# Kernel tuning notes

Hardware: AMD Instinct MI355X
Metric: run time of the kernel (lower is better)

## Reference

```python
import jax, jax.numpy as jnp
import numpy as np

PS = 8          # patch size
E = 8           # experts per layer
L = 2           # PCE layers
F = 4           # fourier frequencies -> pos channels = 2+4F = 18
TEMP = 1.0
GROUPS = 4
B, H, W, CS, NCLS = 64, 128, 128, 8, 100
P = (H // PS) * (W // PS)
N = B * P
CAP = int(np.ceil(1.25 * N / E))  # expert capacity
POSC = 2 + 4 * F


def conv3x3(x, w):
    return jax.lax.conv_general_dilated(x, w, (1, 1), 'SAME',
                                        dimension_numbers=('NCHW', 'OIHW', 'NCHW'))


def patchify(x, ps):
    b, c, h, w = x.shape
    hp, wp = h // ps, w // ps
    t = x.reshape(b, c, hp, ps, wp, ps).transpose(0, 2, 4, 1, 3, 5)
    return t.reshape(b * hp * wp, c, ps, ps), hp, wp


def unpatchify(t, b, hp, wp):
    n, c, ph, pw = t.shape
    return t.reshape(b, hp, wp, c, ph, pw).transpose(0, 3, 1, 4, 2, 5).reshape(b, c, hp * ph, wp * pw)


def fourier_pos(h, w, f):
    yy, xx = jnp.meshgrid(jnp.linspace(-1., 1., h), jnp.linspace(-1., 1., w), indexing='ij')
    feats = [yy, xx]
    for k in range(f):
        fr = jnp.pi * (2.0 ** k)
        feats += [jnp.sin(fr * yy), jnp.cos(fr * yy), jnp.sin(fr * xx), jnp.cos(fr * xx)]
    return jnp.stack(feats, 0)  # [2+4F, H, W]


def group_norm(x, s, b, groups=GROUPS, eps=1e-5):
    n, c, h, w = x.shape
    xg = x.reshape(n, groups, c // groups, h, w)
    mu = xg.mean((2, 3, 4), keepdims=True)
    var = xg.var((2, 3, 4), keepdims=True)
    xg = (xg - mu) / jnp.sqrt(var + eps)
    return xg.reshape(n, c, h, w) * s[None, :, None, None] + b[None, :, None, None]


def setup_inputs():
    key = jax.random.key(0)
    ks = jax.random.split(key, 8)
    return {
        'X': jax.random.normal(ks[0], (B, 3, H, W), jnp.float32),
        'stem_w': jax.random.normal(ks[1], (CS, 3, 3, 3), jnp.float32) * 0.1,
        'stem_scale': jnp.ones((CS,), jnp.float32),
        'stem_bias': jnp.zeros((CS,), jnp.float32),
        'gate_w': jax.random.normal(ks[2], (L, POSC, E), jnp.float32) * 0.1,
        'gate_b': jnp.zeros((L, E), jnp.float32),
        'exp_w': jax.random.normal(ks[3], (L, E, CS, CS, 3, 3), jnp.float32) * 0.05,
        'exp_b': jnp.zeros((L, E, CS), jnp.float32),
        'gn_scale': jnp.ones((L, CS), jnp.float32),
        'gn_bias': jnp.zeros((L, CS), jnp.float32),
        'head_w1': jax.random.normal(ks[4], (CS, 4 * CS), jnp.float32) * 0.1,
        'head_b1': jnp.zeros((4 * CS,), jnp.float32),
        'head_w2': jax.random.normal(ks[5], (4 * CS, NCLS), jnp.float32) * 0.1,
        'head_b2': jnp.zeros((NCLS,), jnp.float32),
    }


def reference(X, stem_w, stem_scale, stem_bias, gate_w, gate_b, exp_w, exp_b,
              gn_scale, gn_bias, head_w1, head_b1, head_w2, head_b2):
    b = X.shape[0]
    # stem: conv + (folded) BN affine + SiLU
    x = jax.nn.silu(conv3x3(X, stem_w) * stem_scale[None, :, None, None]
                    + stem_bias[None, :, None, None])
    tokens, hp, wp = patchify(x, PS)                       # [N, CS, PS, PS]
    pos = fourier_pos(x.shape[2], x.shape[3], F)           # [POSC, H, W]
    pos_p, _, _ = patchify(pos[None], PS)                  # [P, POSC, PS, PS]
    pos_pool = jnp.tile(pos_p.mean((2, 3)), (b, 1))        # [N, POSC]

    tot_z = jnp.float32(0.)
    tot_imb = jnp.float32(0.)
    for l in range(L):
        logits = pos_pool @ gate_w[l] + gate_b[l]          # [N, E]
        probs = jax.nn.softmax(logits / TEMP, axis=-1)
        tot_z = tot_z + jnp.mean(jax.nn.logsumexp(logits, axis=-1) ** 2)
        e_idx = jnp.argmax(probs, axis=-1)                 # top-1 expert per token
        oh = jax.nn.one_hot(e_idx, E, dtype=jnp.float32)
        slot = (jnp.sum(jnp.cumsum(oh, axis=0) * oh, axis=1) - 1.).astype(jnp.int32)
        keep = slot < CAP
        frac = jnp.mean(oh * keep[:, None].astype(jnp.float32), axis=0)
        tot_imb = tot_imb + E * jnp.sum(jnp.mean(probs, axis=0) * frac)
        gate = jnp.take_along_axis(probs, e_idx[:, None], axis=1)[:, 0] * keep.astype(probs.dtype)
        e_safe = jnp.where(keep, e_idx, E)                 # OOB index -> dropped
        einp = jnp.zeros((E, CAP) + tokens.shape[1:], tokens.dtype)
        einp = einp.at[e_safe, slot].set(tokens, mode='drop')   # dispatch gather
        eout = jax.vmap(lambda xi, wi, bi: jax.nn.silu(conv3x3(xi, wi)
                        + bi[None, :, None, None]))(einp, exp_w[l], exp_b[l])
        out = eout[e_idx, jnp.minimum(slot, CAP - 1)] * gate[:, None, None, None]
        if l == L - 1:
            x = group_norm(unpatchify(out, b, hp, wp), gn_scale[l], gn_bias[l])
        else:
            tokens = group_norm(out, gn_scale[l], gn_bias[l])

    pooled = x.mean((2, 3))                                # AdaptiveAvgPool2d(1)+flatten
    h1 = jax.nn.gelu(pooled @ head_w1 + head_b1)
    logits_out = h1 @ head_w2 + head_b2
    return logits_out, tot_z, tot_imb
```

## Files before the change

kernel.cpp:

```cpp
#include <hip/hip_runtime.h>
#include <math.h>

#define CAPV 2560

typedef __bf16 bf16x8 __attribute__((ext_vector_type(8)));
typedef float f32x4 __attribute__((ext_vector_type(4)));

__device__ __forceinline__ float wave_sum64(float v) {
#pragma unroll
  for (int o = 32; o; o >>= 1) v += __shfl_xor(v, o, 64);
  return v;
}

__device__ __forceinline__ float silu_f(float t) {
  return t * __builtin_amdgcn_rcpf(1.f + __expf(-t));
}

__global__ __launch_bounds__(256) void routing_kernel(
    const float* __restrict__ gate_w, const float* __restrict__ gate_b,
    const float* __restrict__ stem_w, const float* __restrict__ stem_sc,
    const float* __restrict__ exp_w,
    int* __restrict__ route_e, float* __restrict__ route_gate,
    int* __restrict__ route_cpre, int* __restrict__ route_Ce,
    __bf16* __restrict__ stemPack, __bf16* __restrict__ expPack,
    float* __restrict__ d_scalars) {
  const int tid = threadIdx.x;
  if (blockIdx.x > 0) {
    int le = blockIdx.x - 1;
    for (int i = tid; i < 1536; i += 256) {
      int c = i >> 9, rem = i & 511, ln = rem >> 3, j = rem & 7;
      int k = c * 32 + ((ln >> 4) << 3) + j;
      int cl = ln & 15;
      int tap = k >> 3, ci = k & 7;
      int dy = tap >> 2, dx = tap & 3;
      float v = 0.f;
      if (cl < 8 && dx < 3)
        v = exp_w[((le * 8 + cl) * 8 + ci) * 9 + dy * 3 + dx];
      expPack[le * 1536 + i] = (__bf16)v;
    }
    return;
  }
  for (int i = tid; i < 1536; i += 256) {
    int c = i >> 9, rem = i & 511, ln = rem >> 3, j = rem & 7;
    int k = c * 32 + ((ln >> 4) << 3) + j;
    int cl = ln & 15;
    int tap = k >> 3, ci = k & 7;
    int dy = tap >> 2, dx = tap & 3;
    float v = 0.f;
    if (cl < 8 && dx < 3 && ci < 3)
      v = stem_w[(cl * 3 + ci) * 9 + dy * 3 + dx] * stem_sc[cl];
    stemPack[i] = (__bf16)v;
  }

  __shared__ float tS[128][4], tC[128][4];
  __shared__ float sS8[16][4], sC8[16][4];
  if (tid < 128) {
    float yv = -1.f + (2.f / 127.f) * (float)tid;
#pragma unroll
    for (int k = 0; k < 4; ++k) {
      float fr = 3.14159265358979323846f * (float)(1 << k);
      tS[tid][k] = sinf(fr * yv);
      tC[tid][k] = cosf(fr * yv);
    }
  }
  __syncthreads();
  if (tid < 64) {
    int g8 = tid >> 2, k = tid & 3;
    float s = 0.f, c = 0.f;
#pragma unroll
    for (int r = 0; r < 8; ++r) {
      s += tS[g8 * 8 + r][k];
      c += tC[g8 * 8 + r][k];
    }
    sS8[g8][k] = s * 0.125f;
    sC8[g8][k] = c * 0.125f;
  }
  __syncthreads();

  const int p = tid;
  const int lane = p & 63, wv = p >> 6;
  const int hp = p >> 4, wp = p & 15;

  float pool[18];
  pool[0] = -1.f + (2.f / 127.f) * ((float)(hp * 8) + 3.5f);
  pool[1] = -1.f + (2.f / 127.f) * ((float)(wp * 8) + 3.5f);
#pragma unroll
  for (int k = 0; k < 4; ++k) {
    pool[2 + 4 * k] = sS8[hp][k];
    pool[3 + 4 * k] = sC8[hp][k];
    pool[4 + 4 * k] = sS8[wp][k];
    pool[5 + 4 * k] = sC8[wp][k];
  }

  __shared__ float sWP[4][8];
  __shared__ float sWZ[4];
  __shared__ int sWCnt[4][8];
  __shared__ float sMeanP[8], sFrac[8];
  __shared__ float sAcc[2];
  if (p == 0) { sAcc[0] = 0.f; sAcc[1] = 0.f; }

  for (int l = 0; l < 2; ++l) {
    float logit[8];
#pragma unroll
    for (int e = 0; e < 8; ++e) logit[e] = gate_b[l * 8 + e];
#pragma unroll
    for (int c = 0; c < 18; ++c) {
      float pl = pool[c];
#pragma unroll
      for (int e = 0; e < 8; ++e)
        logit[e] = fmaf(pl, gate_w[(l * 18 + c) * 8 + e], logit[e]);
    }
    float mxv = logit[0]; int em = 0;
#pragma unroll
    for (int e = 1; e < 8; ++e)
      if (logit[e] > mxv) { mxv = logit[e]; em = e; }
    float pr[8]; float se = 0.f;
#pragma unroll
    for (int e = 0; e < 8; ++e) { pr[e] = expf(logit[e] - mxv); se += pr[e]; }
    float inv = 1.f / se;
#pragma unroll
    for (int e = 0; e < 8; ++e) pr[e] *= inv;
    float lse = mxv + logf(se);
    float gate_val = inv;

    unsigned long long meq[8];
#pragma unroll
    for (int e = 0; e < 8; ++e) meq[e] = __ballot(em == e);
    unsigned long long mm = meq[0];
#pragma unroll
    for (int e = 1; e < 8; ++e) mm = (em == e) ? meq[e] : mm;
    unsigned long long below = (2ull << lane) - 1ull;
    int cpre_w = (int)__popcll(mm & below);
    if (lane < 8) {
      unsigned long long t = meq[0];
#pragma unroll
      for (int e = 1; e < 8; ++e) t = (lane == e) ? meq[e] : t;
      sWCnt[wv][lane] = (int)__popcll(t);
    }
    float z2 = wave_sum64(lse * lse);
    if (lane == 0) sWZ[wv] = z2;
#pragma unroll
    for (int e = 0; e < 8; ++e) {
      float s = wave_sum64(pr[e]);
      if (lane == 0) sWP[wv][e] = s;
    }
    __syncthreads();

    int cpre = cpre_w;
#pragma unroll
    for (int w2 = 0; w2 < 4; ++w2)
      if (w2 < wv) cpre += sWCnt[w2][em];

    route_e[l * 256 + p] = em;
    route_gate[l * 256 + p] = gate_val;
    route_cpre[l * 256 + p] = cpre;

    if (p < 8) {
      int ce = sWCnt[0][p] + sWCnt[1][p] + sWCnt[2][p] + sWCnt[3][p];
      route_Ce[l * 8 + p] = ce;
      int kept = 0;
      for (int bb = 0; bb < 64; ++bb) {
        int r = CAPV - bb * ce;
        r = r < 0 ? 0 : r;
        kept += (r < ce ? r : ce);
      }
      sFrac[p] = (float)kept * (1.f / 16384.f);
      sMeanP[p] = (sWP[0][p] + sWP[1][p] + sWP[2][p] + sWP[3][p]) * (1.f / 256.f);
    }
    __syncthreads();
    if (p == 0) {
      float s = 0.f;
#pragma unroll
      for (int e = 0; e < 8; ++e) s += sMeanP[e] * sFrac[e];
      sAcc[1] += 8.f * s;
      sAcc[0] += (sWZ[0] + sWZ[1] + sWZ[2] + sWZ[3]) * (1.f / 256.f);
    }
    __syncthreads();
  }
  if (p == 0) { d_scalars[0] = sAcc[0]; d_scalars[1] = sAcc[1]; }
}

__global__ __launch_bounds__(256) void token_kernel(
    const float* __restrict__ X,
    const __bf16* __restrict__ stemPack, const float* __restrict__ stem_bi,
    const __bf16* __restrict__ expPack, const float* __restrict__ exp_b,
    const float* __restrict__ gn_s, const float* __restrict__ gn_b,
    const int* __restrict__ route_e, const float* __restrict__ route_gate,
    const int* __restrict__ route_cpre, const int* __restrict__ route_Ce,
    float* __restrict__ blk_sums) {
  const int g = blockIdx.x;
  const int b = g >> 6, r6 = g & 63;
  const int hp = r6 >> 2, wq = r6 & 3;
  const int tid = threadIdx.x;
  const int w = tid >> 6, lane = tid & 63;
  const int p = hp * 16 + wq * 4 + w;

  const int col = lane & 15;
  const int gq = lane >> 4;
  const int ay = (lane & 15) >> 3;
  const int ax = lane & 7;
  const int dy_ = (gq >> 1) + 1, dx_ = (gq & 1) * 4 + 1;

  __shared__ __align__(16) __bf16 sH[10][36][8];
  __shared__ __align__(16) __bf16 sT[4][10][12][8];
  __shared__ float sRed[4][12];

  const int e0 = __builtin_amdgcn_readfirstlane(route_e[p]);
  const int e1 = __builtin_amdgcn_readfirstlane(route_e[256 + p]);
  const float gp0 = route_gate[p], gp1 = route_gate[256 + p];
  const int cp0 = route_cpre[p], cp1 = route_cpre[256 + p];
  const int Ce0 = route_Ce[e0], Ce1 = route_Ce[8 + e1];
  const float gate0 = (col < 8 && b * Ce0 + cp0 <= CAPV) ? gp0 : 0.f;
  const float gate1 = (col < 8 && b * Ce1 + cp1 <= CAPV) ? gp1 : 0.f;
  const int le0 = e0, le1 = 8 + e1;
  const bf16x8* sp = (const bf16x8*)stemPack;
  const bf16x8* bp0 = (const bf16x8*)(expPack + le0 * 1536);
  const bf16x8* bp1 = (const bf16x8*)(expPack + le1 * 1536);
  bf16x8 SB0 = sp[lane], SB1 = sp[64 + lane], SB2 = sp[128 + lane];
  bf16x8 B00 = bp0[lane], B01 = bp0[64 + lane], B02 = bp0[128 + lane];
  bf16x8 B10 = bp1[lane], B11 = bp1[64 + lane], B12 = bp1[128 + lane];

  {
    float4 z4 = {0.f, 0.f, 0.f, 0.f};
    float4* h4 = (float4*)&sH[0][0][0];
#pragma unroll
    for (int i = 0; i < 2; ++i) {
      int idx = tid + i * 256;
      if (idx < 360) h4[idx] = z4;
    }
  }
  if (lane < 56) {
    int row, c2;
    if (lane < 12) { row = 0; c2 = lane; }
    else if (lane < 24) { row = 9; c2 = lane - 12; }
    else { int q = lane - 24; row = 1 + (q >> 2); int m = q & 3; c2 = (m == 0) ? 0 : 8 + m; }
    int4 z = {0, 0, 0, 0};
    *(int4*)&sT[w][row][c2][0] = z;
  }
  __syncthreads();

  const int gy0 = hp * 8 - 1, gx0 = wq * 32 - 1;
#pragma unroll
  for (int k = 0; k < 4; ++k) {
    int i = tid + k * 256;
    if (i < 1020) {
      int ci = i / 340, rem = i - ci * 340;
      int r = rem / 34, c = rem - r * 34;
      int gy = gy0 + r, gx = gx0 + c;
      if (gy >= 0 && gy < 128 && gx >= 0 && gx < 128)
        sH[r][c][ci] = (__bf16)X[((b * 3 + ci) * 128 + gy) * 128 + gx];
    }
  }
  __syncthreads();

  {
    const float bias = stem_bi[col & 7];
    f32x4 d0 = {bias, bias, bias, bias};
    f32x4 d1 = d0, d2 = d0, d3 = d0;
#pragma unroll
    for (int c = 0; c < 3; ++c) {
      const __bf16* ab = &sH[ay + c][w * 8 + ax + gq][0];
      bf16x8 A0 = *(const bf16x8*)(ab);
      bf16x8 A1 = *(const bf16x8*)(ab + 576);
      bf16x8 A2 = *(const bf16x8*)(ab + 1152);
      bf16x8 A3 = *(const bf16x8*)(ab + 1728);
      bf16x8 Bc = (c == 0) ? SB0 : (c == 1) ? SB1 : SB2;
      d0 = __builtin_amdgcn_mfma_f32_16x16x32_bf16(A0, Bc, d0, 0, 0, 0);
      d1 = __builtin_amdgcn_mfma_f32_16x16x32_bf16(A1, Bc, d1, 0, 0, 0);
      d2 = __builtin_amdgcn_mfma_f32_16x16x32_bf16(A2, Bc, d2, 0, 0, 0);
      d3 = __builtin_amdgcn_mfma_f32_16x16x32_bf16(A3, Bc, d3, 0, 0, 0);
    }
    if (col < 8) {
#pragma unroll
      for (int rg = 0; rg < 4; ++rg) {
        f32x4 dr = (rg == 0) ? d0 : (rg == 1) ? d1 : (rg == 2) ? d2 : d3;
#pragma unroll
        for (int r = 0; r < 4; ++r) {
          float t = silu_f(dr[r]);
          sT[w][rg * 2 + dy_][dx_ + r][col] = (__bf16)t;
        }
      }
    }
  }

  const __bf16* abase = &sT[w][ay][ax + gq][0];
  const float bias0 = exp_b[le0 * 8 + (col & 7)];
  const float bias1 = exp_b[le1 * 8 + (col & 7)];
  const float sgs0 = gn_s[col & 7], sgb0 = gn_b[col & 7];

  float v1s, v1q;
  {
    f32x4 a0 = {bias0, bias0, bias0, bias0};
    f32x4 a1 = a0, a2 = a0, a3 = a0;
#pragma unroll
    for (int c = 0; c < 3; ++c) {
      bf16x8 A0 = *(const bf16x8*)(abase + (0 * 192 + c * 96));
      bf16x8 A1 = *(const bf16x8*)(abase + (1 * 192 + c * 96));
      bf16x8 A2 = *(const bf16x8*)(abase + (2 * 192 + c * 96));
      bf16x8 A3 = *(const bf16x8*)(abase + (3 * 192 + c * 96));
      bf16x8 Bc = (c == 0) ? B00 : (c == 1) ? B01 : B02;
      a0 = __builtin_amdgcn_mfma_f32_16x16x32_bf16(A0, Bc, a0, 0, 0, 0);
      a1 = __builtin_amdgcn_mfma_f32_16x16x32_bf16(A1, Bc, a1, 0, 0, 0);
      a2 = __builtin_amdgcn_mfma_f32_16x16x32_bf16(A2, Bc, a2, 0, 0, 0);
      a3 = __builtin_amdgcn_mfma_f32_16x16x32_bf16(A3, Bc, a3, 0, 0, 0);
    }
    float v[16];
    float s = 0.f, q = 0.f;
#pragma unroll
    for (int rg = 0; rg < 4; ++rg) {
      f32x4 ar = (rg == 0) ? a0 : (rg == 1) ? a1 : (rg == 2) ? a2 : a3;
#pragma unroll
      for (int r = 0; r < 4; ++r) {
        float t = silu_f(ar[r]) * gate0;
        v[rg * 4 + r] = t;
        s += t;
        q += t * t;
      }
    }
    s += __shfl_xor(s, 16, 64); q += __shfl_xor(q, 16, 64);
    s += __shfl_xor(s, 32, 64); q += __shfl_xor(q, 32, 64);
    s += __shfl_xor(s, 1, 64);  q += __shfl_xor(q, 1, 64);
    float mu = s * (1.f / 128.f);
    float var = q * (1.f / 128.f) - mu * mu;
    float inv = rsqrtf(var + 1e-5f);
    float sc2 = inv * sgs0;
    float bi2 = fmaf(-mu, sc2, sgb0);
    if (col < 8) {
#pragma unroll
      for (int rg = 0; rg < 4; ++rg)
#pragma unroll
        for (int r = 0; r < 4; ++r) {
          float n = fmaf(v[rg * 4 + r], sc2, bi2);
          sT[w][rg * 2 + dy_][dx_ + r][col] = (__bf16)n;
        }
    }
  }
  {
    f32x4 a0 = {bias1, bias1, bias1, bias1};
    f32x4 a1 = a0, a2 = a0, a3 = a0;
#pragma unroll
    for (int c = 0; c < 3; ++c) {
      bf16x8 A0 = *(const bf16x8*)(abase + (0 * 192 + c * 96));
      bf16x8 A1 = *(const bf16x8*)(abase + (1 * 192 + c * 96));
      bf16x8 A2 = *(const bf16x8*)(abase + (2 * 192 + c * 96));
      bf16x8 A3 = *(const bf16x8*)(abase + (3 * 192 + c * 96));
      bf16x8 Bc = (c == 0) ? B10 : (c == 1) ? B11 : B12;
      a0 = __builtin_amdgcn_mfma_f32_16x16x32_bf16(A0, Bc, a0, 0, 0, 0);
      a1 = __builtin_amdgcn_mfma_f32_16x16x32_bf16(A1, Bc, a1, 0, 0, 0);
      a2 = __builtin_amdgcn_mfma_f32_16x16x32_bf16(A2, Bc, a2, 0, 0, 0);
      a3 = __builtin_amdgcn_mfma_f32_16x16x32_bf16(A3, Bc, a3, 0, 0, 0);
    }
    float s = 0.f, q = 0.f;
#pragma unroll
    for (int rg = 0; rg < 4; ++rg) {
      f32x4 ar = (rg == 0) ? a0 : (rg == 1) ? a1 : (rg == 2) ? a2 : a3;
#pragma unroll
      for (int r = 0; r < 4; ++r) {
        float t = silu_f(ar[r]) * gate1;
        s += t;
        q += t * t;
      }
    }
    s += __shfl_xor(s, 16, 64); q += __shfl_xor(q, 16, 64);
    s += __shfl_xor(s, 32, 64); q += __shfl_xor(q, 32, 64);
    v1s = s;
    v1q = q + __shfl_xor(q, 1, 64);
  }

  if (lane < 8) sRed[w][lane] = v1s;
  if (lane < 8 && !(lane & 1)) sRed[w][8 + (lane >> 1)] = v1q;
  __syncthreads();
  if (tid < 12)
    blk_sums[(size_t)g * 12 + tid] =
        sRed[0][tid] + sRed[1][tid] + sRed[2][tid] + sRed[3][tid];
}

__global__ __launch_bounds__(64) void finish_kernel(
    const float* __restrict__ blk_sums,
    const float* __restrict__ gn_s, const float* __restrict__ gn_b,
    const float* __restrict__ w1, const float* __restrict__ b1,
    const float* __restrict__ w2, const float* __restrict__ b2,
    float* __restrict__ out) {
  const int b = blockIdx.x;
  const int lane = threadIdx.x;

  const float4* s4 = (const float4*)(blk_sums + (size_t)(b * 64 + lane) * 12);
  float4 a0 = s4[0], a1 = s4[1], a2 = s4[2];
  float l0[12] = {a0.x, a0.y, a0.z, a0.w, a1.x, a1.y, a1.z, a1.w,
                  a2.x, a2.y, a2.z, a2.w};
#pragma unroll
  for (int j = 0; j < 12; ++j) l0[j] = wave_sum64(l0[j]);

  float pooled[8];
#pragma unroll
  for (int c = 0; c < 8; ++c) {
    int gg = c >> 1;
    float mean_c = l0[c] * (1.f / 16384.f);
    float mug = (l0[2 * gg] + l0[2 * gg + 1]) * (1.f / 32768.f);
    float var = l0[8 + gg] * (1.f / 32768.f) - mug * mug;
    pooled[c] = fmaf((mean_c - mug) * rsqrtf(var + 1e-5f), gn_s[8 + c], gn_b[8 + c]);
  }

  __shared__ float sH1[32];
  if (lane < 32) {
    float h = b1[lane];
#pragma unroll
    for (int c = 0; c < 8; ++c) h = fmaf(pooled[c], w1[c * 32 + lane], h);
    float t = 0.7978845608028654f * fmaf(0.044715f * h * h, h, h);
    sH1[lane] = 0.5f * h * (1.f + tanhf(t));
  }
  __syncthreads();
  for (int o = lane; o < 100; o += 64) {
    float v = b2[o];
#pragma unroll
    for (int j = 0; j < 32; ++j) v = fmaf(sH1[j], w2[j * 100 + o], v);
    out[b * 100 + o] = v;
  }
}

extern "C" void kernel_launch(void* const* d_in, const int* in_sizes, int n_in,
                              void* d_out, int out_size, void* d_ws, size_t ws_size,
                              hipStream_t stream) {
  const float* X       = (const float*)d_in[0];
  const float* stem_w  = (const float*)d_in[1];
  const float* stem_sc = (const float*)d_in[2];
  const float* stem_bi = (const float*)d_in[3];
  const float* gate_w  = (const float*)d_in[4];
  const float* gate_b  = (const float*)d_in[5];
  const float* exp_w   = (const float*)d_in[6];
  const float* exp_b   = (const float*)d_in[7];
  const float* gn_s    = (const float*)d_in[8];
  const float* gn_b    = (const float*)d_in[9];
  const float* w1      = (const float*)d_in[10];
  const float* b1      = (const float*)d_in[11];
  const float* w2      = (const float*)d_in[12];
  const float* b2      = (const float*)d_in[13];
  float* out = (float*)d_out;

  char* ws = (char*)d_ws;
  int* route_e      = (int*)(ws + 0);
  int* route_cpre   = (int*)(ws + 2048);
  int* route_Ce     = (int*)(ws + 4096);
  float* route_gate = (float*)(ws + 4160);
  __bf16* stemPack  = (__bf16*)(ws + 8192);
  __bf16* expPack   = (__bf16*)(ws + 16384);
  float* blk_sums   = (float*)(ws + 65536);

  routing_kernel<<<17, 256, 0, stream>>>(gate_w, gate_b, stem_w, stem_sc, exp_w,
                                         route_e, route_gate, route_cpre,
                                         route_Ce, stemPack, expPack, out + 6400);
  token_kernel<<<4096, 256, 0, stream>>>(X, stemPack, stem_bi, expPack, exp_b,
                                         gn_s, gn_b, route_e, route_gate,
                                         route_cpre, route_Ce, blk_sums);
  finish_kernel<<<64, 64, 0, stream>>>(blk_sums, gn_s, gn_b, w1, b1, w2, b2,
                                       out);
}
```

Before: 52.14 us.

## Enlarge token blocks to 2x4 patches to share input halo loads

Each token-kernel block now covers a 2x4 tile of patches with 8 waves (512 threads) instead of a 1x4 strip with 4 waves. The shared input halo grows from 10 to 18 rows, so vertically adjacent patches share boundary rows and fewer redundant global loads of X are issued. The grid halves, and the finish kernel reads 32 partial sums per image instead of 64. In exchange, blocks use more LDS and are larger, which may reduce occupancy or scheduling flexibility.

```diff
diff --git a/kernel.cpp b/kernel.cpp
--- a/kernel.cpp
+++ b/kernel.cpp
@@ -180,7 +180,7 @@
   if (p == 0) { d_scalars[0] = sAcc[0]; d_scalars[1] = sAcc[1]; }
 }
 
-__global__ __launch_bounds__(256) void token_kernel(
+__global__ __launch_bounds__(512) void token_kernel(
     const float* __restrict__ X,
     const __bf16* __restrict__ stemPack, const float* __restrict__ stem_bi,
     const __bf16* __restrict__ expPack, const float* __restrict__ exp_b,
@@ -189,11 +189,12 @@
     const int* __restrict__ route_cpre, const int* __restrict__ route_Ce,
     float* __restrict__ blk_sums) {
   const int g = blockIdx.x;
-  const int b = g >> 6, r6 = g & 63;
-  const int hp = r6 >> 2, wq = r6 & 3;
+  const int b = g >> 5, t5 = g & 31;
+  const int tr = t5 >> 2, tc = t5 & 3;
   const int tid = threadIdx.x;
   const int w = tid >> 6, lane = tid & 63;
-  const int p = hp * 16 + wq * 4 + w;
+  const int pr = tr * 2 + (w >> 2), pc = tc * 4 + (w & 3);
+  const int p = pr * 16 + pc;
 
   const int col = lane & 15;
   const int gq = lane >> 4;
@@ -201,9 +202,9 @@
   const int ax = lane & 7;
   const int dy_ = (gq >> 1) + 1, dx_ = (gq & 1) * 4 + 1;
 
-  __shared__ __align__(16) __bf16 sH[10][36][8];
-  __shared__ __align__(16) __bf16 sT[4][10][12][8];
-  __shared__ float sRed[4][12];
+  __shared__ __align__(16) __bf16 sH[18][36][8];
+  __shared__ __align__(16) __bf16 sT[8][10][12][8];
+  __shared__ float sRed[8][12];
 
   const int e0 = __builtin_amdgcn_readfirstlane(route_e[p]);
   const int e1 = __builtin_amdgcn_readfirstlane(route_e[256 + p]);
@@ -225,8 +226,8 @@
     float4* h4 = (float4*)&sH[0][0][0];
 #pragma unroll
     for (int i = 0; i < 2; ++i) {
-      int idx = tid + i * 256;
-      if (idx < 360) h4[idx] = z4;
+      int idx = tid + i * 512;
+      if (idx < 648) h4[idx] = z4;
     }
   }
   if (lane < 56) {
@@ -239,12 +240,12 @@
   }
   __syncthreads();
 
-  const int gy0 = hp * 8 - 1, gx0 = wq * 32 - 1;
+  const int gy0 = tr * 16 - 1, gx0 = tc * 32 - 1;
 #pragma unroll
   for (int k = 0; k < 4; ++k) {
-    int i = tid + k * 256;
-    if (i < 1020) {
-      int ci = i / 340, rem = i - ci * 340;
+    int i = tid + k * 512;
+    if (i < 1836) {
+      int ci = i / 612, rem = i - ci * 612;
       int r = rem / 34, c = rem - r * 34;
       int gy = gy0 + r, gx = gx0 + c;
       if (gy >= 0 && gy < 128 && gx >= 0 && gx < 128)
@@ -253,13 +254,15 @@
   }
   __syncthreads();
 
+  const int hy0 = (w >> 2) * 8;
+  const int hx0 = (w & 3) * 8;
   {
     const float bias = stem_bi[col & 7];
     f32x4 d0 = {bias, bias, bias, bias};
     f32x4 d1 = d0, d2 = d0, d3 = d0;
 #pragma unroll
     for (int c = 0; c < 3; ++c) {
-      const __bf16* ab = &sH[ay + c][w * 8 + ax + gq][0];
+      const __bf16* ab = &sH[hy0 + ay + c][hx0 + ax + gq][0];
       bf16x8 A0 = *(const bf16x8*)(ab);
       bf16x8 A1 = *(const bf16x8*)(ab + 576);
       bf16x8 A2 = *(const bf16x8*)(ab + 1152);
@@ -370,9 +373,12 @@
   if (lane < 8) sRed[w][lane] = v1s;
   if (lane < 8 && !(lane & 1)) sRed[w][8 + (lane >> 1)] = v1q;
   __syncthreads();
-  if (tid < 12)
-    blk_sums[(size_t)g * 12 + tid] =
-        sRed[0][tid] + sRed[1][tid] + sRed[2][tid] + sRed[3][tid];
+  if (tid < 12) {
+    float bs = 0.f;
+#pragma unroll
+    for (int w2 = 0; w2 < 8; ++w2) bs += sRed[w2][tid];
+    blk_sums[(size_t)g * 12 + tid] = bs;
+  }
 }
 
 __global__ __launch_bounds__(64) void finish_kernel(
@@ -384,10 +390,14 @@
   const int b = blockIdx.x;
   const int lane = threadIdx.x;
 
-  const float4* s4 = (const float4*)(blk_sums + (size_t)(b * 64 + lane) * 12);
-  float4 a0 = s4[0], a1 = s4[1], a2 = s4[2];
-  float l0[12] = {a0.x, a0.y, a0.z, a0.w, a1.x, a1.y, a1.z, a1.w,
-                  a2.x, a2.y, a2.z, a2.w};
+  float l0[12] = {0.f, 0.f, 0.f, 0.f, 0.f, 0.f, 0.f, 0.f, 0.f, 0.f, 0.f, 0.f};
+  if (lane < 32) {
+    const float4* s4 = (const float4*)(blk_sums + (size_t)(b * 32 + lane) * 12);
+    float4 a0 = s4[0], a1 = s4[1], a2 = s4[2];
+    l0[0] = a0.x; l0[1] = a0.y; l0[2] = a0.z; l0[3] = a0.w;
+    l0[4] = a1.x; l0[5] = a1.y; l0[6] = a1.z; l0[7] = a1.w;
+    l0[8] = a2.x; l0[9] = a2.y; l0[10] = a2.z; l0[11] = a2.w;
+  }
 #pragma unroll
   for (int j = 0; j < 12; ++j) l0[j] = wave_sum64(l0[j]);
 
@@ -449,7 +459,7 @@
   routing_kernel<<<17, 256, 0, stream>>>(gate_w, gate_b, stem_w, stem_sc, exp_w,
                                          route_e, route_gate, route_cpre,
                                          route_Ce, stemPack, expPack, out + 6400);
-  token_kernel<<<4096, 256, 0, stream>>>(X, stemPack, stem_bi, expPack, exp_b,
+  token_kernel<<<2048, 512, 0, stream>>>(X, stemPack, stem_bi, expPack, exp_b,
                                          gn_s, gn_b, route_e, route_gate,
                                          route_cpre, route_Ce, blk_sums);
   finish_kernel<<<64, 64, 0, stream>>>(blk_sums, gn_s, gn_b, w1, b1, w2, b2,
```

Result: no change. 51.55 us (-1.1%).
